# Optimization experiments

Hardware: AMD Instinct MI355X
Metric: run time of the kernel (lower is better)

Reference implementation:

```python
import jax, jax.numpy as jnp
import numpy as np

BATCH = 2048
DIM = 100000
K = 16


def setup_inputs() -> dict:
    key = jax.random.key(0)
    k1, k2, k3 = jax.random.split(key, 3)
    inputs = jax.random.uniform(k1, (BATCH, DIM), dtype=jnp.float32)
    w = jax.random.normal(k2, (DIM, 1), dtype=jnp.float32)
    v = jax.random.normal(k3, (DIM, K), dtype=jnp.float32)
    return {"inputs": inputs, "w": w, "v": v}


def reference(inputs, w, v):
    # linear term: [batch]
    logits = jnp.squeeze(inputs @ w, axis=-1)
    # 2nd-order FM interaction via square-of-sum minus sum-of-square trick
    square_of_sum = jnp.square(inputs @ v)              # [batch, k]
    sum_of_square = jnp.square(inputs) @ jnp.square(v)  # [batch, k]
    logits = logits + 0.5 * jnp.sum(square_of_sum - sum_of_square, axis=1)
    return logits
```

## Files before the change

kernel.cpp:

```cpp
#include <hip/hip_runtime.h>
#include <hip/hip_bf16.h>

#define BATCH 2048
#define DIM   100000
#define STEPS 3125
#define NSPLIT 8
#define NTILES 49
#define ROWTILES 128

typedef float f32x4  __attribute__((ext_vector_type(4)));
typedef short bf16x8 __attribute__((ext_vector_type(8)));

__device__ __forceinline__ short f2bf(float f) {
    return (short)__builtin_bit_cast(unsigned short, __float2bfloat16(f));
}

__global__ __launch_bounds__(128) void fm_pack(
        const float* __restrict__ w, const float* __restrict__ v,
        short* __restrict__ Bv, short* __restrict__ Bc) {
    int t = blockIdx.x * blockDim.x + threadIdx.x;
    if (t >= STEPS * 4) return;
    int j = t >> 2, h = t & 3;
    int d0 = j * 32 + h * 8;
    size_t base = (size_t)j * 512 + (size_t)h * 128;

    short bv[16][8];
    float v2s[8];
    short wbits[8];
    #pragma unroll
    for (int i = 0; i < 8; ++i) {
        const f32x4* vp = (const f32x4*)(v + (size_t)(d0 + i) * 16);
        f32x4 r0 = vp[0], r1 = vp[1], r2 = vp[2], r3 = vp[3];
        float s = 0.f;
        #pragma unroll
        for (int q = 0; q < 4; ++q) {
            s += r0[q]*r0[q] + r1[q]*r1[q] + r2[q]*r2[q] + r3[q]*r3[q];
            bv[q + 0][i]  = f2bf(r0[q]);
            bv[q + 4][i]  = f2bf(r1[q]);
            bv[q + 8][i]  = f2bf(r2[q]);
            bv[q + 12][i] = f2bf(r3[q]);
        }
        v2s[i] = s;
        wbits[i] = f2bf(w[d0 + i]);
    }
    #pragma unroll
    for (int c = 0; c < 16; ++c) {
        bf16x8 o;
        #pragma unroll
        for (int i = 0; i < 8; ++i) o[i] = bv[c][i];
        *(bf16x8*)(Bv + base + c * 8) = o;
    }
    bf16x8 z = (bf16x8)0;
    bf16x8 c0, c1;
    #pragma unroll
    for (int i = 0; i < 8; ++i) { c0[i] = wbits[i]; c1[i] = f2bf(v2s[i]); }
    *(bf16x8*)(Bc + base + 0) = c0;
    *(bf16x8*)(Bc + base + 8) = c1;
    #pragma unroll
    for (int c = 2; c < 16; ++c) *(bf16x8*)(Bc + base + c * 8) = z;
}

__global__ __launch_bounds__(256, 4) void fm_main(
        const float* __restrict__ x,
        const short* __restrict__ Bv, const short* __restrict__ Bc,
        float* __restrict__ P) {
    const int bid     = blockIdx.x;
    const int split   = bid & 7;
    const int rowtile = bid >> 3;
    const int lane = threadIdx.x & 63;
    const int wave = threadIdx.x >> 6;
    const int c = lane & 15;
    const int h = lane >> 4;
    const int xc = (c & 7) << 4;

    const int step_base  = split * 390 + (split < 5 ? split : 5);
    const int tail_steps = 6 + (split < 5 ? 1 : 0);

    __shared__ float lds[2][16 * 256];

    const int col0s = step_base * 32;
    f32x4 stA[4], stB[4];

    f32x4 acc_s = {0.f, 0.f, 0.f, 0.f};
    f32x4 acc_l = {0.f, 0.f, 0.f, 0.f};
    f32x4 acc_q = {0.f, 0.f, 0.f, 0.f};

    auto issue = [&](f32x4 (&st)[4], int t) {
        if (t >= NTILES) return;
        const int ncols = (t < 48) ? 256 : tail_steps * 32;
        const bool ok = lane * 4 < ncols;
        const int colf = col0s + t * 256 + lane * 4;
        #pragma unroll
        for (int R = 0; R < 4; ++R) {
            int r = R * 4 + wave;
            const float* p = x + (size_t)(rowtile * 16 + r) * DIM + colf;
            if (ok) st[R] = *(const f32x4*)p;
        }
    };
    auto writeLDS = [&](int buf, f32x4 (&st)[4], int t) {
        if (t >= NTILES) return;
        const int ncols = (t < 48) ? 256 : tail_steps * 32;
        const bool ok = lane * 4 < ncols;
        #pragma unroll
        for (int R = 0; R < 4; ++R) {
            int r = R * 4 + wave;
            int off = r * 256 + ((((lane * 16) ^ ((r & 7) << 4))) >> 2);
            if (ok) *(f32x4*)&lds[buf][off] = st[R];
        }
    };
    auto compute = [&](int buf, int t) {
        if (t >= NTILES) return;
        const int nsteps = (t < 48) ? 8 : tail_steps;
        const int jbase = step_base + t * 8;
        #pragma unroll
        for (int ss = 0; ss < 2; ++ss) {
            int s = wave * 2 + ss;
            if (s < nsteps) {
                bf16x8 bv = *(const bf16x8*)(Bv + (size_t)(jbase + s) * 512 + h * 128 + c * 8);
                bf16x8 bc = *(const bf16x8*)(Bc + (size_t)(jbase + s) * 512 + h * 128 + c * 8);
                int W = s * 128 + h * 32;
                const float* base = &lds[buf][c * 256];
                f32x4 xa = *(const f32x4*)(base + ((W ^ xc) >> 2));
                f32x4 xb = *(const f32x4*)(base + (((W + 16) ^ xc) >> 2));
                bf16x8 a1, a2;
                #pragma unroll
                for (int i = 0; i < 4; ++i) {
                    a1[i]     = f2bf(xa[i]);
                    a1[i + 4] = f2bf(xb[i]);
                    a2[i]     = f2bf(xa[i] * xa[i]);
                    a2[i + 4] = f2bf(xb[i] * xb[i]);
                }
                acc_s = __builtin_amdgcn_mfma_f32_16x16x32_bf16(a1, bv, acc_s, 0, 0, 0);
                acc_l = __builtin_amdgcn_mfma_f32_16x16x32_bf16(a1, bc, acc_l, 0, 0, 0);
                acc_q = __builtin_amdgcn_mfma_f32_16x16x32_bf16(a2, bc, acc_q, 0, 0, 0);
            }
        }
    };

    issue(stA, 0);
    issue(stB, 1);
    writeLDS(0, stA, 0);
    for (int tt = 0; tt < NTILES; tt += 2) {
        __syncthreads();
        compute(0, tt);
        issue(stA, tt + 2);
        writeLDS(1, stB, tt + 1);
        __syncthreads();
        compute(1, tt + 1);
        issue(stB, tt + 3);
        writeLDS(0, stA, tt + 2);
    }

    __syncthreads();
    float* red = &lds[0][0];
    int rbase = (wave * 64 + lane) * 12;
    #pragma unroll
    for (int i = 0; i < 4; ++i) {
        red[rbase + i]     = acc_s[i];
        red[rbase + 4 + i] = acc_l[i];
        red[rbase + 8 + i] = acc_q[i];
    }
    __syncthreads();
    if (wave == 0) {
        f32x4 s = {0,0,0,0}, l = {0,0,0,0}, q = {0,0,0,0};
        #pragma unroll
        for (int wv = 0; wv < 4; ++wv) {
            const float* rp = &red[(wv * 64 + lane) * 12];
            #pragma unroll
            for (int i = 0; i < 4; ++i) {
                s[i] += rp[i]; l[i] += rp[4 + i]; q[i] += rp[8 + i];
            }
        }
        #pragma unroll
        for (int r = 0; r < 4; ++r) {
            size_t row = (size_t)rowtile * 16 + h * 4 + r;
            float* Pp = P + (row * NSPLIT + split) * 18;
            Pp[c] = s[r];
            if (c == 0) Pp[16] = l[r];
            if (c == 1) Pp[17] = q[r];
        }
    }
}

__global__ __launch_bounds__(64) void fm_reduce(const float* __restrict__ P,
                                                float* __restrict__ out) {
    int b = blockIdx.x;
    int lane = threadIdx.x;
    float r[18];
    if (lane < NSPLIT) {
        const float* q = P + ((size_t)b * NSPLIT + lane) * 18;
        #pragma unroll
        for (int i = 0; i < 18; ++i) r[i] = q[i];
    } else {
        #pragma unroll
        for (int i = 0; i < 18; ++i) r[i] = 0.f;
    }
    #pragma unroll
    for (int off = 4; off > 0; off >>= 1) {
        #pragma unroll
        for (int i = 0; i < 18; ++i) r[i] += __shfl_xor(r[i], off, 64);
    }
    if (lane == 0) {
        float acc = r[16] - 0.5f * r[17];
        #pragma unroll
        for (int k = 0; k < 16; ++k) acc += 0.5f * r[k] * r[k];
        out[b] = acc;
    }
}

extern "C" void kernel_launch(void* const* d_in, const int* in_sizes, int n_in,
                              void* d_out, int out_size, void* d_ws, size_t ws_size,
                              hipStream_t stream) {
    const float* x = (const float*)d_in[0];
    const float* w = (const float*)d_in[1];
    const float* v = (const float*)d_in[2];
    float* out = (float*)d_out;

    char* ws = (char*)d_ws;
    short* Bv = (short*)(ws);
    short* Bc = (short*)(ws + 3200000);
    float* P  = (float*)(ws + 6400000);

    fm_pack<<<(STEPS * 4 + 127) / 128, 128, 0, stream>>>(w, v, Bv, Bc);
    fm_main<<<NSPLIT * ROWTILES, 256, 0, stream>>>(x, Bv, Bc, P);
    fm_reduce<<<BATCH, 64, 0, stream>>>(P, out);
}
```

Baseline: 178.2 us.

## Stage x as bf16 in LDS with larger tiles and prefetched B fragments

```diff
diff --git a/kernel.cpp b/kernel.cpp
--- a/kernel.cpp
+++ b/kernel.cpp
@@ -5,59 +5,78 @@
 #define DIM   100000
 #define STEPS 3125
 #define NSPLIT 8
-#define NTILES 49
+#define NTILES 25
 #define ROWTILES 128
 
 typedef float f32x4  __attribute__((ext_vector_type(4)));
 typedef short bf16x8 __attribute__((ext_vector_type(8)));
+typedef short bf16x4 __attribute__((ext_vector_type(4)));
 
 __device__ __forceinline__ short f2bf(float f) {
     return (short)__builtin_bit_cast(unsigned short, __float2bfloat16(f));
 }
-
-__global__ __launch_bounds__(128) void fm_pack(
+__device__ __forceinline__ float bf2f(short s) {
+    unsigned u = ((unsigned)(unsigned short)s) << 16;
+    return __builtin_bit_cast(float, u);
+}
+
+__global__ __launch_bounds__(256) void fm_pack(
         const float* __restrict__ w, const float* __restrict__ v,
         short* __restrict__ Bv, short* __restrict__ Bc) {
-    int t = blockIdx.x * blockDim.x + threadIdx.x;
-    if (t >= STEPS * 4) return;
-    int j = t >> 2, h = t & 3;
-    int d0 = j * 32 + h * 8;
-    size_t base = (size_t)j * 512 + (size_t)h * 128;
-
-    short bv[16][8];
-    float v2s[8];
-    short wbits[8];
-    #pragma unroll
-    for (int i = 0; i < 8; ++i) {
-        const f32x4* vp = (const f32x4*)(v + (size_t)(d0 + i) * 16);
-        f32x4 r0 = vp[0], r1 = vp[1], r2 = vp[2], r3 = vp[3];
-        float s = 0.f;
-        #pragma unroll
-        for (int q = 0; q < 4; ++q) {
-            s += r0[q]*r0[q] + r1[q]*r1[q] + r2[q]*r2[q] + r3[q]*r3[q];
-            bv[q + 0][i]  = f2bf(r0[q]);
-            bv[q + 4][i]  = f2bf(r1[q]);
-            bv[q + 8][i]  = f2bf(r2[q]);
-            bv[q + 12][i] = f2bf(r3[q]);
-        }
-        v2s[i] = s;
-        wbits[i] = f2bf(w[d0 + i]);
-    }
-    #pragma unroll
-    for (int c = 0; c < 16; ++c) {
-        bf16x8 o;
-        #pragma unroll
-        for (int i = 0; i < 8; ++i) o[i] = bv[c][i];
-        *(bf16x8*)(Bv + base + c * 8) = o;
-    }
-    bf16x8 z = (bf16x8)0;
-    bf16x8 c0, c1;
-    #pragma unroll
-    for (int i = 0; i < 8; ++i) { c0[i] = wbits[i]; c1[i] = f2bf(v2s[i]); }
-    *(bf16x8*)(Bc + base + 0) = c0;
-    *(bf16x8*)(Bc + base + 8) = c1;
-    #pragma unroll
-    for (int c = 2; c < 16; ++c) *(bf16x8*)(Bc + base + c * 8) = z;
+    __shared__ float vt[128][17];
+    __shared__ float wt[128];
+    const int t  = threadIdx.x;
+    const int jb = blockIdx.x * 4;
+    const int d_base = jb * 32;
+    const int nd = (DIM - d_base < 128) ? (DIM - d_base) : 128;
+
+    #pragma unroll
+    for (int q = 0; q < 2; ++q) {
+        int e = t * 8 + q * 4;
+        if (e < nd * 16) {
+            f32x4 r = *(const f32x4*)(v + (size_t)d_base * 16 + e);
+            #pragma unroll
+            for (int i = 0; i < 4; ++i) vt[(e + i) >> 4][(e + i) & 15] = r[i];
+        }
+    }
+    if (t < 32) {
+        int d = t * 4;
+        if (d < nd) {
+            f32x4 r = *(const f32x4*)(w + d_base + d);
+            #pragma unroll
+            for (int i = 0; i < 4; ++i) if (d + i < nd) wt[d + i] = r[i];
+        }
+    }
+    __syncthreads();
+
+    const int jp = t >> 6;
+    const int j  = jb + jp;
+    if (j >= STEPS) return;
+    const int rem = t & 63;
+    const int h = rem >> 4, c = rem & 15;
+    const int dl0 = jp * 32 + h * 8;
+    size_t off = (size_t)j * 512 + h * 128 + c * 8;
+
+    bf16x8 ov, oc;
+    #pragma unroll
+    for (int i = 0; i < 8; ++i) ov[i] = f2bf(vt[dl0 + i][c]);
+    *(bf16x8*)(Bv + off) = ov;
+
+    if (c == 0) {
+        #pragma unroll
+        for (int i = 0; i < 8; ++i) oc[i] = f2bf(wt[dl0 + i]);
+    } else if (c == 1) {
+        #pragma unroll
+        for (int i = 0; i < 8; ++i) {
+            float s = 0.f;
+            #pragma unroll
+            for (int k = 0; k < 16; ++k) { float vv = vt[dl0 + i][k]; s += vv * vv; }
+            oc[i] = f2bf(s);
+        }
+    } else {
+        oc = (bf16x8)0;
+    }
+    *(bf16x8*)(Bc + off) = oc;
 }
 
 __global__ __launch_bounds__(256, 4) void fm_main(
@@ -71,88 +90,104 @@
     const int wave = threadIdx.x >> 6;
     const int c = lane & 15;
     const int h = lane >> 4;
-    const int xc = (c & 7) << 4;
 
     const int step_base  = split * 390 + (split < 5 ? split : 5);
     const int tail_steps = 6 + (split < 5 ? 1 : 0);
 
-    __shared__ float lds[2][16 * 256];
+    __shared__ short lds[2][16 * 512];
 
     const int col0s = step_base * 32;
-    f32x4 stA[4], stB[4];
+    f32x4 st[4][2];
+    bf16x8 bvr[4], bcr[4];
 
     f32x4 acc_s = {0.f, 0.f, 0.f, 0.f};
     f32x4 acc_l = {0.f, 0.f, 0.f, 0.f};
     f32x4 acc_q = {0.f, 0.f, 0.f, 0.f};
 
-    auto issue = [&](f32x4 (&st)[4], int t) {
+    auto issue = [&](int t) {
         if (t >= NTILES) return;
-        const int ncols = (t < 48) ? 256 : tail_steps * 32;
-        const bool ok = lane * 4 < ncols;
-        const int colf = col0s + t * 256 + lane * 4;
+        const int ncols = (t < 24) ? 512 : tail_steps * 32;
+        const int colf = col0s + t * 512;
         #pragma unroll
         for (int R = 0; R < 4; ++R) {
-            int r = R * 4 + wave;
+            int r = wave * 4 + R;
             const float* p = x + (size_t)(rowtile * 16 + r) * DIM + colf;
-            if (ok) st[R] = *(const f32x4*)p;
-        }
-    };
-    auto writeLDS = [&](int buf, f32x4 (&st)[4], int t) {
+            if (lane * 4 < ncols)
+                st[R][0] = __builtin_nontemporal_load((const f32x4*)(p + lane * 4));
+            if (256 + lane * 4 < ncols)
+                st[R][1] = __builtin_nontemporal_load((const f32x4*)(p + 256 + lane * 4));
+        }
+    };
+    auto writeLDS = [&](int buf, int t) {
         if (t >= NTILES) return;
-        const int ncols = (t < 48) ? 256 : tail_steps * 32;
-        const bool ok = lane * 4 < ncols;
+        const int ncols = (t < 24) ? 512 : tail_steps * 32;
         #pragma unroll
         for (int R = 0; R < 4; ++R) {
-            int r = R * 4 + wave;
-            int off = r * 256 + ((((lane * 16) ^ ((r & 7) << 4))) >> 2);
-            if (ok) *(f32x4*)&lds[buf][off] = st[R];
+            int r = wave * 4 + R;
+            int swz = (r & 7) << 4;
+            char* base = (char*)&lds[buf][0];
+            if (lane * 4 < ncols) {
+                bf16x4 o; 
+                #pragma unroll
+                for (int i = 0; i < 4; ++i) o[i] = f2bf(st[R][0][i]);
+                *(bf16x4*)(base + (r * 1024 + ((lane * 8) ^ swz))) = o;
+            }
+            if (256 + lane * 4 < ncols) {
+                bf16x4 o;
+                #pragma unroll
+                for (int i = 0; i < 4; ++i) o[i] = f2bf(st[R][1][i]);
+                *(bf16x4*)(base + (r * 1024 + ((512 + lane * 8) ^ swz))) = o;
+            }
+        }
+    };
+    auto loadB = [&](int t) {
+        if (t >= NTILES) return;
+        int jbase = step_base + t * 16;
+        #pragma unroll
+        for (int ss = 0; ss < 4; ++ss) {
+            int s = jbase + wave * 4 + ss;
+            if (s > STEPS - 1) s = STEPS - 1;
+            size_t off = (size_t)s * 512 + h * 128 + c * 8;
+            bvr[ss] = *(const bf16x8*)(Bv + off);
+            bcr[ss] = *(const bf16x8*)(Bc + off);
         }
     };
     auto compute = [&](int buf, int t) {
-        if (t >= NTILES) return;
-        const int nsteps = (t < 48) ? 8 : tail_steps;
-        const int jbase = step_base + t * 8;
-        #pragma unroll
-        for (int ss = 0; ss < 2; ++ss) {
-            int s = wave * 2 + ss;
+        const int nsteps = (t < 24) ? 16 : tail_steps;
+        const char* base = (const char*)&lds[buf][0];
+        const int swz = (c & 7) << 4;
+        #pragma unroll
+        for (int ss = 0; ss < 4; ++ss) {
+            int s = wave * 4 + ss;
             if (s < nsteps) {
-                bf16x8 bv = *(const bf16x8*)(Bv + (size_t)(jbase + s) * 512 + h * 128 + c * 8);
-                bf16x8 bc = *(const bf16x8*)(Bc + (size_t)(jbase + s) * 512 + h * 128 + c * 8);
-                int W = s * 128 + h * 32;
-                const float* base = &lds[buf][c * 256];
-                f32x4 xa = *(const f32x4*)(base + ((W ^ xc) >> 2));
-                f32x4 xb = *(const f32x4*)(base + (((W + 16) ^ xc) >> 2));
-                bf16x8 a1, a2;
+                bf16x8 a1 = *(const bf16x8*)(base + (c * 1024 + ((s * 64 + h * 16) ^ swz)));
+                bf16x8 a2;
                 #pragma unroll
-                for (int i = 0; i < 4; ++i) {
-                    a1[i]     = f2bf(xa[i]);
-                    a1[i + 4] = f2bf(xb[i]);
-                    a2[i]     = f2bf(xa[i] * xa[i]);
-                    a2[i + 4] = f2bf(xb[i] * xb[i]);
+                for (int i = 0; i < 8; ++i) {
+                    float f = bf2f(a1[i]);
+                    a2[i] = f2bf(f * f);
                 }
-                acc_s = __builtin_amdgcn_mfma_f32_16x16x32_bf16(a1, bv, acc_s, 0, 0, 0);
-                acc_l = __builtin_amdgcn_mfma_f32_16x16x32_bf16(a1, bc, acc_l, 0, 0, 0);
-                acc_q = __builtin_amdgcn_mfma_f32_16x16x32_bf16(a2, bc, acc_q, 0, 0, 0);
-            }
-        }
-    };
-
-    issue(stA, 0);
-    issue(stB, 1);
-    writeLDS(0, stA, 0);
-    for (int tt = 0; tt < NTILES; tt += 2) {
+                acc_s = __builtin_amdgcn_mfma_f32_16x16x32_bf16(a1, bvr[ss], acc_s, 0, 0, 0);
+                acc_l = __builtin_amdgcn_mfma_f32_16x16x32_bf16(a1, bcr[ss], acc_l, 0, 0, 0);
+                acc_q = __builtin_amdgcn_mfma_f32_16x16x32_bf16(a2, bcr[ss], acc_q, 0, 0, 0);
+            }
+        }
+    };
+
+    loadB(0);
+    issue(0);
+    writeLDS(0, 0);
+    issue(1);
+    for (int t = 0; t < NTILES; ++t) {
         __syncthreads();
-        compute(0, tt);
-        issue(stA, tt + 2);
-        writeLDS(1, stB, tt + 1);
-        __syncthreads();
-        compute(1, tt + 1);
-        issue(stB, tt + 3);
-        writeLDS(0, stA, tt + 2);
+        compute(t & 1, t);
+        loadB(t + 1);
+        writeLDS((t + 1) & 1, t + 1);
+        issue(t + 2);
     }
 
     __syncthreads();
-    float* red = &lds[0][0];
+    float* red = (float*)&lds[0][0];
     int rbase = (wave * 64 + lane) * 12;
     #pragma unroll
     for (int i = 0; i < 4; ++i) {
@@ -221,7 +256,7 @@
     short* Bc = (short*)(ws + 3200000);
     float* P  = (float*)(ws + 6400000);
 
-    fm_pack<<<(STEPS * 4 + 127) / 128, 128, 0, stream>>>(w, v, Bv, Bc);
+    fm_pack<<<(STEPS + 3) / 4, 256, 0, stream>>>(w, v, Bv, Bc);
     fm_main<<<NSPLIT * ROWTILES, 256, 0, stream>>>(x, Bv, Bc, P);
     fm_reduce<<<BATCH, 64, 0, stream>>>(P, out);
 }
```

Result: faster. 158.5 us (-11.1%).
